# Performance work log

Measured on AMD Instinct MI355X. Metric: run time of the kernel, lower is better.

The kernel has to match this reference:

```python
import jax, jax.numpy as jnp
import numpy as np

B_SZ, L_SEQ, ENC_IN = 8, 1024, 32
D_MODEL, D_INNER, D_STATE, D_CONV, DT_RANK = 256, 512, 16, 4, 16
N_LAYERS, D_FF, C_OUT = 2, 1024, 1


def setup_inputs() -> dict:
    key = jax.random.key(0)
    ks = jax.random.split(key, 16)
    s = 0.02
    inp = {}
    inp["x"] = jax.random.normal(ks[0], (B_SZ, L_SEQ, ENC_IN), jnp.float32)
    inp["in_w"] = jax.random.normal(ks[1], (D_MODEL, ENC_IN), jnp.float32) * s
    inp["in_b"] = jnp.zeros((D_MODEL,), jnp.float32)
    inp["in_proj_w"] = jax.random.normal(ks[2], (N_LAYERS, 2 * D_INNER, D_MODEL), jnp.float32) * s
    inp["conv_w"] = jax.random.normal(ks[3], (N_LAYERS, D_INNER, D_CONV), jnp.float32) * 0.1
    inp["conv_b"] = jnp.zeros((N_LAYERS, D_INNER), jnp.float32)
    inp["x_proj_w"] = jax.random.normal(ks[4], (N_LAYERS, DT_RANK + 2 * D_STATE, D_INNER), jnp.float32) * s
    inp["dt_w"] = jax.random.normal(ks[5], (N_LAYERS, D_INNER, DT_RANK), jnp.float32) * (DT_RANK ** -0.5)
    dt = jax.random.uniform(ks[6], (N_LAYERS, D_INNER), jnp.float32, 1e-3, 0.1)
    inp["dt_b"] = dt + jnp.log(-jnp.expm1(-dt))  # inverse softplus
    inp["A_log"] = jnp.tile(jnp.log(jnp.arange(1, D_STATE + 1, dtype=jnp.float32)), (N_LAYERS, D_INNER, 1))
    inp["D_skip"] = jnp.ones((N_LAYERS, D_INNER), jnp.float32)
    inp["out_proj_w"] = jax.random.normal(ks[7], (N_LAYERS, D_MODEL, D_INNER), jnp.float32) * s
    inp["p1_w"] = jax.random.normal(ks[8], (D_FF, D_MODEL), jnp.float32) * s
    inp["p1_b"] = jnp.zeros((D_FF,), jnp.float32)
    inp["p2_w"] = jax.random.normal(ks[9], (C_OUT, D_FF), jnp.float32) * s
    inp["p2_b"] = jnp.zeros((C_OUT,), jnp.float32)
    return inp


def causal_dw_conv(x, w, b):
    # x: [b, l, d], w: [d, k] depthwise, left-pad for causality
    xc = jax.lax.conv_general_dilated(
        x.transpose(0, 2, 1), w[:, None, :], (1,), [(D_CONV - 1, 0)],
        feature_group_count=D_INNER, dimension_numbers=("NCH", "OIH", "NCH"))
    return (xc + b[None, :, None]).transpose(0, 2, 1)


def selective_scan(u, dt, A, Bm, Cm):
    # u, dt: [b, l, d]; Bm, Cm: [b, l, n]; A: [d, n]
    def step(h, inp):
        u_t, dt_t, B_t, C_t = inp  # [b,d],[b,d],[b,n],[b,n]
        dA = jnp.exp(dt_t[..., None] * A)                      # [b,d,n]
        dBu = dt_t[..., None] * B_t[:, None, :] * u_t[..., None]
        h = dA * h + dBu
        y = jnp.einsum("bdn,bn->bd", h, C_t)
        return h, y
    h0 = jnp.zeros((u.shape[0], D_INNER, D_STATE), u.dtype)
    xs = (u.transpose(1, 0, 2), dt.transpose(1, 0, 2),
          Bm.transpose(1, 0, 2), Cm.transpose(1, 0, 2))
    _, ys = jax.lax.scan(step, h0, xs)
    return ys.transpose(1, 0, 2)  # [b, l, d]


def mamba_block(h, ipw, cw, cb, xpw, dtw, dtb, Alog, Dp, opw):
    xz = jnp.einsum("bld,ed->ble", h, ipw)          # [b,l,2*d_inner]
    xi, z = jnp.split(xz, 2, axis=-1)
    xc = jax.nn.silu(causal_dw_conv(xi, cw, cb))     # [b,l,d_inner]
    xdbl = jnp.einsum("bld,ed->ble", xc, xpw)        # [b,l,dt_rank+2n]
    dt_lo = xdbl[..., :DT_RANK]
    Bm = xdbl[..., DT_RANK:DT_RANK + D_STATE]
    Cm = xdbl[..., DT_RANK + D_STATE:]
    dt = jax.nn.softplus(jnp.einsum("blr,dr->bld", dt_lo, dtw) + dtb)
    A = -jnp.exp(Alog)
    y = selective_scan(xc, dt, A, Bm, Cm) + xc * Dp
    y = y * jax.nn.silu(z)
    return jnp.einsum("bld,ed->ble", y, opw)


def reference(x, in_w, in_b, in_proj_w, conv_w, conv_b, x_proj_w, dt_w, dt_b,
              A_log, D_skip, out_proj_w, p1_w, p1_b, p2_w, p2_b):
    h = jnp.einsum("bli,di->bld", x, in_w) + in_b
    for i in range(N_LAYERS):
        h = mamba_block(h, in_proj_w[i], conv_w[i], conv_b[i], x_proj_w[i],
                        dt_w[i], dt_b[i], A_log[i], D_skip[i], out_proj_w[i])
    h = h[:, -1, :]  # last timestep
    h = jax.nn.gelu(jnp.einsum("bd,fd->bf", h, p1_w) + p1_b, approximate=False)
    return jnp.einsum("bf,cf->bc", h, p2_w) + p2_b
```

## Files before the change

### kernel.cpp

```cpp
#include <hip/hip_runtime.h>
#include <math.h>


static constexpr int L_SEQ = 1024;
static constexpr int M_ROWS = 8 * 1024;
static constexpr int NCHUNK = 32;
static constexpr int TCHUNK = 32;

typedef unsigned short u16;
typedef unsigned short u16x8 __attribute__((ext_vector_type(8)));
typedef unsigned short u16x4 __attribute__((ext_vector_type(4)));
typedef short bf16x8 __attribute__((ext_vector_type(8)));
typedef float f32x4 __attribute__((ext_vector_type(4)));

__device__ __forceinline__ float silu_f(float x) { return x / (1.f + __expf(-x)); }
__device__ __forceinline__ float softplus_f(float x) {
  return (x > 20.f) ? x : log1pf(__expf(x));
}
__device__ __forceinline__ u16 f2bf(float f) {
  unsigned u = __builtin_bit_cast(unsigned, f);
  u += 0x7FFFu + ((u >> 16) & 1u);
  return (u16)(u >> 16);
}
__device__ __forceinline__ float bf2f(u16 v) {
  return __builtin_bit_cast(float, (unsigned)v << 16);
}

__device__ __forceinline__ void gll16(const u16* g, u16* l) {
  __builtin_amdgcn_global_load_lds(
      (const __attribute__((address_space(1))) void*)g,
      (__attribute__((address_space(3))) void*)l, 16, 0, 0);
}

template<int BM,int BN,int BK,int EPI,int OUTBF>
__global__ __launch_bounds__(256)
void gemm_db(const u16* __restrict__ A, int lda,
             const u16* __restrict__ W, int ldw,
             const float* __restrict__ bias,
             void* __restrict__ Cp, int ldc,
             int N, int K)
{
  constexpr int KS = BK / 32;
  constexpr int CA = BK / 8;
  constexpr int NCH_A = (BM / 64) * CA;
  constexpr int NCH_B = (BN / 64) * CA;
  constexpr int TI = BM / 2 / 16;
  constexpr int TJ = BN / 2 / 16;

  __shared__ u16 As[2][BM * BK];
  __shared__ u16 Ws[2][BN * BK];

  const int tid = threadIdx.x;
  const int lane = tid & 63;
  const int wv = tid >> 6;
  const int wy = wv >> 1, wx = wv & 1;
  const int rb = wy * (BM / 2);
  const int cb = wx * (BN / 2);
  const int lr = lane & 15, lq = lane >> 4;
  const int bm = blockIdx.x * BM;
  const int bn = blockIdx.y * BN;

  f32x4 acc[TI][TJ];
#pragma unroll
  for (int i = 0; i < TI; ++i)
#pragma unroll
    for (int j = 0; j < TJ; ++j) acc[i][j] = (f32x4){0.f, 0.f, 0.f, 0.f};

  auto stage = [&](int k0, int buf) {
#pragma unroll
    for (int w = wv; w < NCH_A + NCH_B; w += 4) {
      if (w < NCH_A) {
        const int rh = w / CA, lqw = w % CA;
        gll16(A + (size_t)(bm + rh * 64 + lane) * lda + k0 + lqw * 8,
              &As[buf][(lqw * BM + rh * 64) * 8]);
      } else {
        const int w2 = w - NCH_A;
        const int rh = w2 / CA, lqw = w2 % CA;
        gll16(W + (size_t)(bn + rh * 64 + lane) * ldw + k0 + lqw * 8,
              &Ws[buf][(lqw * BN + rh * 64) * 8]);
      }
    }
  };

  stage(0, 0);
  int cur = 0;
  for (int k0 = 0; k0 < K; k0 += BK) {
    __syncthreads();
    if (k0 + BK < K) stage(k0 + BK, cur ^ 1);

#pragma unroll
    for (int ks = 0; ks < KS; ++ks) {
      const int lqc = ks * 4 + lq;
      bf16x8 af[TI], bf[TJ];
#pragma unroll
      for (int i = 0; i < TI; ++i)
        af[i] = *reinterpret_cast<const bf16x8*>(
                  &As[cur][(lqc * BM + rb + i * 16 + lr) * 8]);
#pragma unroll
      for (int j = 0; j < TJ; ++j)
        bf[j] = *reinterpret_cast<const bf16x8*>(
                  &Ws[cur][(lqc * BN + cb + j * 16 + lr) * 8]);
#pragma unroll
      for (int i = 0; i < TI; ++i)
#pragma unroll
        for (int j = 0; j < TJ; ++j)
          acc[i][j] = __builtin_amdgcn_mfma_f32_16x16x32_bf16(af[i], bf[j], acc[i][j], 0, 0, 0);
    }
    cur ^= 1;
  }

#pragma unroll
  for (int i = 0; i < TI; ++i) {
#pragma unroll
    for (int j = 0; j < TJ; ++j) {
      const int col = bn + cb + j * 16 + lr;
      if (col >= N) continue;
#pragma unroll
      for (int r = 0; r < 4; ++r) {
        const int row = bm + rb + i * 16 + lq * 4 + r;
        float c = acc[i][j][r];
        if (EPI == 1) c += bias[col];
        if (EPI == 2) { if (col < 512) c = softplus_f(c + bias[col]); }
        if (OUTBF) ((u16*)Cp)[(size_t)row * ldc + col] = f2bf(c);
        else       ((float*)Cp)[(size_t)row * ldc + col] = c;
      }
    }
  }
}

__global__ __launch_bounds__(512)
void prep(const float* __restrict__ x, const float* __restrict__ in_w,
          const float* __restrict__ in_b,
          const float* __restrict__ ipw, const float* __restrict__ opw,
          const float* __restrict__ dtw, const float* __restrict__ xpw,
          u16* __restrict__ x16, u16* __restrict__ opw16,
          u16* __restrict__ ipw16l1, u16* __restrict__ wc1,
          float* __restrict__ bias1, u16* __restrict__ wc)
{
  const int blk = blockIdx.x;
  if (blk < 384) {
    const float* src; u16* dst; int base;
    if (blk < 128)      { src = x;            dst = x16;     base = blk; }
    else if (blk < 256) { src = opw;          dst = opw16;   base = blk - 128; }
    else                { src = ipw + 262144; dst = ipw16l1; base = blk - 256; }
    const int i = (base * 512 + threadIdx.x) * 4;
    float4 v = *reinterpret_cast<const float4*>(src + i);
    u16x4 o;
    o[0] = f2bf(v.x); o[1] = f2bf(v.y); o[2] = f2bf(v.z); o[3] = f2bf(v.w);
    *reinterpret_cast<u16x4*>(dst + i) = o;
  } else if (blk < 448) {
    const int t = threadIdx.x;
    const int n = (blk - 384) * 16 + (t >> 5);
    const int enc = t & 31;
    const float* iprow = ipw + (size_t)n * 256;
    float v = 0.f;
#pragma unroll 8
    for (int j = 0; j < 256; ++j) v = fmaf(iprow[j], in_w[j * 32 + enc], v);
    wc1[n * 32 + enc] = f2bf(v);
    if (enc == 0) {
      float bv = 0.f;
      for (int j = 0; j < 256; ++j) bv = fmaf(iprow[j], in_b[j], bv);
      bias1[n] = bv;
    }
  } else {
    const int idx = blk - 448;
    const int layer = idx / 640;
    const int n = idx % 640;
    const int k = threadIdx.x;
    const float* xp = xpw + (size_t)layer * 48 * 512;
    float v = 0.f;
    if (n < 512) {
      const float* dw = dtw + (size_t)layer * 512 * 16 + n * 16;
#pragma unroll
      for (int r = 0; r < 16; ++r) v = fmaf(dw[r], xp[r * 512 + k], v);
    } else if (n < 544) {
      v = xp[(16 + (n - 512)) * 512 + k];
    }
    wc[((size_t)layer * 640 + n) * 512 + k] = f2bf(v);
  }
}

__global__ __launch_bounds__(512)
void conv_silu(const u16* __restrict__ xz, const float* __restrict__ cw,
               const float* __restrict__ cb, u16* __restrict__ xc)
{
  const int b = blockIdx.x;
  const int l0 = blockIdx.y * 32;
  const int d = threadIdx.x;

  const float w0 = cw[d * 4 + 0], w1 = cw[d * 4 + 1];
  const float w2 = cw[d * 4 + 2], w3 = cw[d * 4 + 3];
  const float bias = cb[d];

  const size_t base = ((size_t)b * L_SEQ) * 1024 + d;
  float xm3 = (l0 >= 3) ? bf2f(xz[base + (size_t)(l0 - 3) * 1024]) : 0.f;
  float xm2 = (l0 >= 2) ? bf2f(xz[base + (size_t)(l0 - 2) * 1024]) : 0.f;
  float xm1 = (l0 >= 1) ? bf2f(xz[base + (size_t)(l0 - 1) * 1024]) : 0.f;

#pragma unroll 4
  for (int i = 0; i < 32; ++i) {
    const int l = l0 + i;
    const float x0 = bf2f(xz[base + (size_t)l * 1024]);
    const float v = bias + w0 * xm3 + w1 * xm2 + w2 * xm1 + w3 * x0;
    xc[((size_t)b * L_SEQ + l) * 512 + d] = f2bf(silu_f(v));
    xm3 = xm2; xm2 = xm1; xm1 = x0;
  }
}

__global__ __launch_bounds__(256)
void scan_passA(const float* __restrict__ xo, const u16* __restrict__ u,
                const float* __restrict__ Alog,
                float* __restrict__ Ac, float* __restrict__ Bc)
{
  const int b = blockIdx.x;
  const int d = blockIdx.y * 256 + threadIdx.x;
  const int c = blockIdx.z;
  const int t0 = c * TCHUNK;

  __shared__ float sB[TCHUNK][16];
#pragma unroll
  for (int r = 0; r < TCHUNK * 16; r += 256) {
    const int e = threadIdx.x + r;
    const int t = e >> 4, n = e & 15;
    sB[t][n] = xo[((size_t)b * L_SEQ + t0 + t) * 544 + 512 + n];
  }
  __syncthreads();

  float A[16], h[16], p[16];
  const float* al = Alog + d * 16;
#pragma unroll
  for (int n = 0; n < 16; ++n) { A[n] = -__expf(al[n]); h[n] = 0.f; p[n] = 1.f; }

#pragma unroll 2
  for (int t = 0; t < TCHUNK; ++t) {
    const size_t row = (size_t)b * L_SEQ + t0 + t;
    const float dtv = xo[row * 544 + d];
    const float uv  = bf2f(u[row * 512 + d]);
    const float cf  = dtv * uv;
    const f32x4* Bq = reinterpret_cast<const f32x4*>(&sB[t][0]);
#pragma unroll
    for (int q = 0; q < 4; ++q) {
      const f32x4 Bv = Bq[q];
#pragma unroll
      for (int k = 0; k < 4; ++k) {
        const int n = q * 4 + k;
        const float dA = __expf(dtv * A[n]);
        p[n] *= dA;
        h[n] = fmaf(dA, h[n], cf * Bv[k]);
      }
    }
  }

  float* ac = Ac + (((size_t)b * NCHUNK + c) * 512 + d) * 16;
  float* bc = Bc + (((size_t)b * NCHUNK + c) * 512 + d) * 16;
#pragma unroll
  for (int q = 0; q < 4; ++q) {
    f32x4 va, vb;
#pragma unroll
    for (int k = 0; k < 4; ++k) { va[k] = p[q * 4 + k]; vb[k] = h[q * 4 + k]; }
    reinterpret_cast<f32x4*>(ac)[q] = va;
    reinterpret_cast<f32x4*>(bc)[q] = vb;
  }
}

__global__ __launch_bounds__(256)
void scan_mid(const float* __restrict__ Ac, const float* __restrict__ Bc,
              float* __restrict__ Hin)
{
  const int gid = blockIdx.x * 256 + threadIdx.x;
  const int b = gid >> 13;
  const int e = gid & 8191;
  float h = 0.f;
  for (int c = 0; c < NCHUNK; ++c) {
    const size_t idx = ((size_t)(b * NCHUNK + c)) * 8192 + e;
    Hin[idx] = h;
    h = fmaf(Ac[idx], h, Bc[idx]);
  }
}

__global__ __launch_bounds__(256)
void scan_passB(const float* __restrict__ xo, const u16* __restrict__ u,
                const u16* __restrict__ xz,
                const float* __restrict__ Alog, const float* __restrict__ Dsk,
                const float* __restrict__ Hin, u16* __restrict__ yg)
{
  const int b = blockIdx.x;
  const int d = blockIdx.y * 256 + threadIdx.x;
  const int c = blockIdx.z;
  const int t0 = c * TCHUNK;

  __shared__ float sB[TCHUNK][16], sC[TCHUNK][16];
#pragma unroll
  for (int r = 0; r < TCHUNK * 16; r += 256) {
    const int e = threadIdx.x + r;
    const int t = e >> 4, n = e & 15;
    const size_t row = (size_t)b * L_SEQ + t0 + t;
    sB[t][n] = xo[row * 544 + 512 + n];
    sC[t][n] = xo[row * 544 + 528 + n];
  }
  __syncthreads();

  float A[16], h[16];
  const float* al = Alog + d * 16;
#pragma unroll
  for (int n = 0; n < 16; ++n) A[n] = -__expf(al[n]);

  const float* hp = Hin + (((size_t)b * NCHUNK + c) * 512 + d) * 16;
#pragma unroll
  for (int q = 0; q < 4; ++q) {
    const f32x4 v = reinterpret_cast<const f32x4*>(hp)[q];
#pragma unroll
    for (int k = 0; k < 4; ++k) h[q * 4 + k] = v[k];
  }

  const float Dv = Dsk[d];

#pragma unroll 2
  for (int t = 0; t < TCHUNK; ++t) {
    const size_t row = (size_t)b * L_SEQ + t0 + t;
    const float dtv = xo[row * 544 + d];
    const float uv  = bf2f(u[row * 512 + d]);
    const float zf  = bf2f(xz[row * 1024 + 512 + d]);
    const float cf  = dtv * uv;
    const f32x4* Bq = reinterpret_cast<const f32x4*>(&sB[t][0]);
    const f32x4* Cq = reinterpret_cast<const f32x4*>(&sC[t][0]);
    float s0 = 0.f, s1 = 0.f, s2 = 0.f, s3 = 0.f;
#pragma unroll
    for (int q = 0; q < 4; ++q) {
      const f32x4 Bv = Bq[q];
      const f32x4 Cv = Cq[q];
#pragma unroll
      for (int k = 0; k < 4; ++k) {
        const int n = q * 4 + k;
        const float dA = __expf(dtv * A[n]);
        h[n] = fmaf(dA, h[n], cf * Bv[k]);
      }
      s0 = fmaf(h[q * 4 + 0], Cv[0], s0);
      s1 = fmaf(h[q * 4 + 1], Cv[1], s1);
      s2 = fmaf(h[q * 4 + 2], Cv[2], s2);
      s3 = fmaf(h[q * 4 + 3], Cv[3], s3);
    }
    const float yv = fmaf(uv, Dv, (s0 + s1) + (s2 + s3));
    yg[row * 512 + d] = f2bf(yv * silu_f(zf));
  }
}

__global__ __launch_bounds__(1024)
void head(const u16* __restrict__ h, const float* __restrict__ p1w,
          const float* __restrict__ p1b, const float* __restrict__ p2w,
          const float* __restrict__ p2b, float* __restrict__ out)
{
  const int b = blockIdx.x;
  const int f = threadIdx.x;

  __shared__ float hl[256];
  if (f < 256) hl[f] = bf2f(h[((size_t)b * L_SEQ + (L_SEQ - 1)) * 256 + f]);
  __syncthreads();

  const float* wr = p1w + (size_t)f * 256;
  float acc = 0.f;
#pragma unroll 8
  for (int k = 0; k < 256; k += 4) {
    float4 wv = *reinterpret_cast<const float4*>(wr + k);
    acc = fmaf(hl[k + 0], wv.x, acc);
    acc = fmaf(hl[k + 1], wv.y, acc);
    acc = fmaf(hl[k + 2], wv.z, acc);
    acc = fmaf(hl[k + 3], wv.w, acc);
  }
  const float xv = acc + p1b[f];
  const float gg = 0.5f * xv * (1.f + erff(xv * 0.70710678118654752f));
  float s = gg * p2w[f];

  s += __shfl_xor(s, 1);
  s += __shfl_xor(s, 2);
  s += __shfl_xor(s, 4);
  s += __shfl_xor(s, 8);
  s += __shfl_xor(s, 16);
  s += __shfl_xor(s, 32);
  __shared__ float red[16];
  if ((f & 63) == 0) red[f >> 6] = s;
  __syncthreads();
  if (f == 0) {
    float t = 0.f;
#pragma unroll
    for (int i = 0; i < 16; ++i) t += red[i];
    out[b] = t + p2b[0];
  }
}

extern "C" void kernel_launch(void* const* d_in, const int* in_sizes, int n_in,
                              void* d_out, int out_size, void* d_ws, size_t ws_size,
                              hipStream_t stream)
{
  const float* x    = (const float*)d_in[0];
  const float* in_w = (const float*)d_in[1];
  const float* in_b = (const float*)d_in[2];
  const float* ipw  = (const float*)d_in[3];
  const float* cw   = (const float*)d_in[4];
  const float* cb   = (const float*)d_in[5];
  const float* xpw  = (const float*)d_in[6];
  const float* dtw  = (const float*)d_in[7];
  const float* dtb  = (const float*)d_in[8];
  const float* Alog = (const float*)d_in[9];
  const float* Dsk  = (const float*)d_in[10];
  const float* opw  = (const float*)d_in[11];
  const float* p1w  = (const float*)d_in[12];
  const float* p1b  = (const float*)d_in[13];
  const float* p2w  = (const float*)d_in[14];
  const float* p2b  = (const float*)d_in[15];

  float* ws = (float*)d_ws;
  u16*   h16  = (u16*)(ws);
  u16*   xz16 = (u16*)(ws + 1048576);
  u16*   xc16 = (u16*)(ws + 5242880);
  float* xo   = ws + 7340032;
  u16*   wc16 = (u16*)(ws + 11796480);
  u16*   wbf  = (u16*)(ws + 12124160);
  float* Ac   = ws + 12660736;
  float* Bc   = ws + 14757888;
  float* Hin  = ws + 16855040;
  u16*   wc1  = (u16*)(ws + 18952192);
  float* bias1 = ws + 18968576;

  u16* x16     = wbf;
  u16* opw16   = wbf + 262144;
  u16* ipw16l1 = wbf + 524288;

  prep<<<1728, 512, 0, stream>>>(x, in_w, in_b, ipw, opw, dtw, xpw,
                                 x16, opw16, ipw16l1, wc1, bias1, wc16);

  {
    gemm_db<64, 128, 32, 1, 1><<<dim3(M_ROWS / 64, 8), 256, 0, stream>>>(
        x16, 32, wc1, 32, bias1, xz16, 1024, 1024, 32);

    conv_silu<<<dim3(8, 32), 512, 0, stream>>>(xz16, cw, cb, xc16);

    gemm_db<64, 128, 64, 2, 0><<<dim3(M_ROWS / 64, 5), 256, 0, stream>>>(
        xc16, 512, wc16, 512, dtb, xo, 544, 544, 512);

    scan_passA<<<dim3(8, 2, NCHUNK), 256, 0, stream>>>(
        xo, xc16, Alog, Ac, Bc);
    scan_mid<<<256, 256, 0, stream>>>(Ac, Bc, Hin);
    scan_passB<<<dim3(8, 2, NCHUNK), 256, 0, stream>>>(
        xo, xc16, xz16, Alog, Dsk, Hin, xc16);

    gemm_db<64, 64, 64, 0, 1><<<dim3(M_ROWS / 64, 4), 256, 0, stream>>>(
        xc16, 512, opw16, 512, nullptr, h16, 256, 256, 512);
  }

  {
    const float* cw_l  = cw  + 512 * 4;
    const float* cb_l  = cb  + 512;
    const float* dtb_l = dtb + 512;
    const float* Al_l  = Alog + 512 * 16;
    const float* Dsk_l = Dsk + 512;
    const u16*   opw_l = opw16 + 256 * 512;
    const u16*   wc_l  = wc16 + 640 * 512;

    gemm_db<64, 128, 64, 0, 1><<<dim3(M_ROWS / 64, 8), 256, 0, stream>>>(
        h16, 256, ipw16l1, 256, nullptr, xz16, 1024, 1024, 256);

    conv_silu<<<dim3(8, 32), 512, 0, stream>>>(xz16, cw_l, cb_l, xc16);

    gemm_db<64, 128, 64, 2, 0><<<dim3(M_ROWS / 64, 5), 256, 0, stream>>>(
        xc16, 512, wc_l, 512, dtb_l, xo, 544, 544, 512);

    scan_passA<<<dim3(8, 2, NCHUNK), 256, 0, stream>>>(
        xo, xc16, Al_l, Ac, Bc);
    scan_mid<<<256, 256, 0, stream>>>(Ac, Bc, Hin);
    scan_passB<<<dim3(8, 2, NCHUNK), 256, 0, stream>>>(
        xo, xc16, xz16, Al_l, Dsk_l, Hin, xc16);

    gemm_db<64, 64, 64, 0, 1><<<dim3(M_ROWS / 64, 4), 256, 0, stream>>>(
        xc16, 512, opw_l, 512, nullptr, h16, 256, 256, 512);
  }

  head<<<8, 1024, 0, stream>>>(h16, p1w, p1b, p2w, p2b, (float*)d_out);
}
```

Baseline: 370.1 us.

## Fuse chunked selective scan passes into one kernel with in-LDS carry propagation

Replaces the three-kernel chunked scan (passA, mid, passB) with one kernel. Each block handles 8 channels across all 32 time chunks: threads compute per-chunk decay products and partial states, store them in shared memory, run the cross-chunk prefix in LDS, then do the output pass. This removes two launches per layer and the global round trip of the Ac/Bc/Hin buffers. In exchange, B/C are read straight from global memory rather than staged in LDS, and per-timestep accesses are now strided across chunks, so coalescing worsens.

Result: faster. 361.1 us (-2.4%).

```diff
diff --git a/kernel.cpp b/kernel.cpp
--- a/kernel.cpp
+++ b/kernel.cpp
@@ -208,23 +208,20 @@
 }
 
 __global__ __launch_bounds__(256)
-void scan_passA(const float* __restrict__ xo, const u16* __restrict__ u,
-                const float* __restrict__ Alog,
-                float* __restrict__ Ac, float* __restrict__ Bc)
+void k_scan(const float* __restrict__ xo, const u16* __restrict__ u,
+            const u16* __restrict__ xz, const float* __restrict__ Alog,
+            const float* __restrict__ Dsk, u16* __restrict__ yg)
 {
   const int b = blockIdx.x;
-  const int d = blockIdx.y * 256 + threadIdx.x;
-  const int c = blockIdx.z;
+  const int d0 = blockIdx.y * 8;
+  const int tid = threadIdx.x;
+  const int dl = tid & 7;
+  const int c = tid >> 3;
+  const int d = d0 + dl;
   const int t0 = c * TCHUNK;
 
-  __shared__ float sB[TCHUNK][16];
-#pragma unroll
-  for (int r = 0; r < TCHUNK * 16; r += 256) {
-    const int e = threadIdx.x + r;
-    const int t = e >> 4, n = e & 15;
-    sB[t][n] = xo[((size_t)b * L_SEQ + t0 + t) * 544 + 512 + n];
-  }
-  __syncthreads();
+  __shared__ float sAg[NCHUNK][8][16];
+  __shared__ float sBg[NCHUNK][8][16];
 
   float A[16], h[16], p[16];
   const float* al = Alog + d * 16;
@@ -237,7 +234,7 @@
     const float dtv = xo[row * 544 + d];
     const float uv  = bf2f(u[row * 512 + d]);
     const float cf  = dtv * uv;
-    const f32x4* Bq = reinterpret_cast<const f32x4*>(&sB[t][0]);
+    const f32x4* Bq = reinterpret_cast<const f32x4*>(&xo[row * 544 + 512]);
 #pragma unroll
     for (int q = 0; q < 4; ++q) {
       const f32x4 Bv = Bq[q];
@@ -251,68 +248,35 @@
     }
   }
 
-  float* ac = Ac + (((size_t)b * NCHUNK + c) * 512 + d) * 16;
-  float* bc = Bc + (((size_t)b * NCHUNK + c) * 512 + d) * 16;
 #pragma unroll
   for (int q = 0; q < 4; ++q) {
     f32x4 va, vb;
 #pragma unroll
     for (int k = 0; k < 4; ++k) { va[k] = p[q * 4 + k]; vb[k] = h[q * 4 + k]; }
-    reinterpret_cast<f32x4*>(ac)[q] = va;
-    reinterpret_cast<f32x4*>(bc)[q] = vb;
-  }
-}
-
-__global__ __launch_bounds__(256)
-void scan_mid(const float* __restrict__ Ac, const float* __restrict__ Bc,
-              float* __restrict__ Hin)
-{
-  const int gid = blockIdx.x * 256 + threadIdx.x;
-  const int b = gid >> 13;
-  const int e = gid & 8191;
-  float h = 0.f;
-  for (int c = 0; c < NCHUNK; ++c) {
-    const size_t idx = ((size_t)(b * NCHUNK + c)) * 8192 + e;
-    Hin[idx] = h;
-    h = fmaf(Ac[idx], h, Bc[idx]);
-  }
-}
-
-__global__ __launch_bounds__(256)
-void scan_passB(const float* __restrict__ xo, const u16* __restrict__ u,
-                const u16* __restrict__ xz,
-                const float* __restrict__ Alog, const float* __restrict__ Dsk,
-                const float* __restrict__ Hin, u16* __restrict__ yg)
-{
-  const int b = blockIdx.x;
-  const int d = blockIdx.y * 256 + threadIdx.x;
-  const int c = blockIdx.z;
-  const int t0 = c * TCHUNK;
-
-  __shared__ float sB[TCHUNK][16], sC[TCHUNK][16];
-#pragma unroll
-  for (int r = 0; r < TCHUNK * 16; r += 256) {
-    const int e = threadIdx.x + r;
-    const int t = e >> 4, n = e & 15;
-    const size_t row = (size_t)b * L_SEQ + t0 + t;
-    sB[t][n] = xo[row * 544 + 512 + n];
-    sC[t][n] = xo[row * 544 + 528 + n];
+    *reinterpret_cast<f32x4*>(&sAg[c][dl][q * 4]) = va;
+    *reinterpret_cast<f32x4*>(&sBg[c][dl][q * 4]) = vb;
   }
   __syncthreads();
 
-  float A[16], h[16];
-  const float* al = Alog + d * 16;
-#pragma unroll
-  for (int n = 0; n < 16; ++n) A[n] = -__expf(al[n]);
-
-  const float* hp = Hin + (((size_t)b * NCHUNK + c) * 512 + d) * 16;
+  if (tid < 128) {
+    const int pd = tid >> 4;
+    const int pn = tid & 15;
+    float hh = 0.f;
+    for (int cc = 0; cc < NCHUNK; ++cc) {
+      const float a  = sAg[cc][pd][pn];
+      const float bb = sBg[cc][pd][pn];
+      sAg[cc][pd][pn] = hh;
+      hh = fmaf(a, hh, bb);
+    }
+  }
+  __syncthreads();
+
 #pragma unroll
   for (int q = 0; q < 4; ++q) {
-    const f32x4 v = reinterpret_cast<const f32x4*>(hp)[q];
+    const f32x4 v = *reinterpret_cast<const f32x4*>(&sAg[c][dl][q * 4]);
 #pragma unroll
     for (int k = 0; k < 4; ++k) h[q * 4 + k] = v[k];
   }
-
   const float Dv = Dsk[d];
 
 #pragma unroll 2
@@ -322,8 +286,8 @@
     const float uv  = bf2f(u[row * 512 + d]);
     const float zf  = bf2f(xz[row * 1024 + 512 + d]);
     const float cf  = dtv * uv;
-    const f32x4* Bq = reinterpret_cast<const f32x4*>(&sB[t][0]);
-    const f32x4* Cq = reinterpret_cast<const f32x4*>(&sC[t][0]);
+    const f32x4* Bq = reinterpret_cast<const f32x4*>(&xo[row * 544 + 512]);
+    const f32x4* Cq = reinterpret_cast<const f32x4*>(&xo[row * 544 + 528]);
     float s0 = 0.f, s1 = 0.f, s2 = 0.f, s3 = 0.f;
 #pragma unroll
     for (int q = 0; q < 4; ++q) {
@@ -416,11 +380,8 @@
   float* xo   = ws + 7340032;
   u16*   wc16 = (u16*)(ws + 11796480);
   u16*   wbf  = (u16*)(ws + 12124160);
-  float* Ac   = ws + 12660736;
-  float* Bc   = ws + 14757888;
-  float* Hin  = ws + 16855040;
-  u16*   wc1  = (u16*)(ws + 18952192);
-  float* bias1 = ws + 18968576;
+  u16*   wc1  = (u16*)(ws + 12517376);
+  float* bias1 = ws + 12533760;
 
   u16* x16     = wbf;
   u16* opw16   = wbf + 262144;
@@ -438,11 +399,7 @@
     gemm_db<64, 128, 64, 2, 0><<<dim3(M_ROWS / 64, 5), 256, 0, stream>>>(
         xc16, 512, wc16, 512, dtb, xo, 544, 544, 512);
 
-    scan_passA<<<dim3(8, 2, NCHUNK), 256, 0, stream>>>(
-        xo, xc16, Alog, Ac, Bc);
-    scan_mid<<<256, 256, 0, stream>>>(Ac, Bc, Hin);
-    scan_passB<<<dim3(8, 2, NCHUNK), 256, 0, stream>>>(
-        xo, xc16, xz16, Alog, Dsk, Hin, xc16);
+    k_scan<<<dim3(8, 64), 256, 0, stream>>>(xo, xc16, xz16, Alog, Dsk, xc16);
 
     gemm_db<64, 64, 64, 0, 1><<<dim3(M_ROWS / 64, 4), 256, 0, stream>>>(
         xc16, 512, opw16, 512, nullptr, h16, 256, 256, 512);
@@ -465,11 +422,7 @@
     gemm_db<64, 128, 64, 2, 0><<<dim3(M_ROWS / 64, 5), 256, 0, stream>>>(
         xc16, 512, wc_l, 512, dtb_l, xo, 544, 544, 512);
 
-    scan_passA<<<dim3(8, 2, NCHUNK), 256, 0, stream>>>(
-        xo, xc16, Al_l, Ac, Bc);
-    scan_mid<<<256, 256, 0, stream>>>(Ac, Bc, Hin);
-    scan_passB<<<dim3(8, 2, NCHUNK), 256, 0, stream>>>(
-        xo, xc16, xz16, Al_l, Dsk_l, Hin, xc16);
+    k_scan<<<dim3(8, 64), 256, 0, stream>>>(xo, xc16, xz16, Al_l, Dsk_l, xc16);
 
     gemm_db<64, 64, 64, 0, 1><<<dim3(M_ROWS / 64, 4), 256, 0, stream>>>(
         xc16, 512, opw_l, 512, nullptr, h16, 256, 256, 512);
```
